# Kernel tuning notes

Hardware: AMD Instinct MI355X
Metric: run time of the kernel (lower is better)

## Reference

```python
import jax, jax.numpy as jnp
import numpy as np

N_NODES = 50000
N_EDGES = 800000
F_DIM = 128
H_DIM = 128


def setup_inputs() -> dict:
    key = jax.random.key(0)
    ks = jax.random.split(key, 14)
    sx = 1.0 / np.sqrt(F_DIM)
    sh = 1.0 / np.sqrt(H_DIM)
    return {
        'x': jax.random.normal(ks[0], (N_NODES, F_DIM), jnp.float32),
        'edge_index': jax.random.randint(ks[1], (2, N_EDGES), 0, N_NODES),
        'edge_weight': jnp.zeros((N_EDGES,), jnp.int32),  # relation ids, all 0 (num_relations=1)
        'h': jax.random.normal(ks[2], (N_NODES, H_DIM), jnp.float32),
        'c': jax.random.normal(ks[3], (N_NODES, H_DIM), jnp.float32),
        # stacked gate params, gate order: i, f, c, o
        'Wx': jax.random.normal(ks[4], (4, F_DIM, H_DIM), jnp.float32) * sx,
        'Wx_root': jax.random.normal(ks[5], (4, F_DIM, H_DIM), jnp.float32) * sx,
        'bx': jax.random.normal(ks[6], (4, H_DIM), jnp.float32) * 0.01,
        'Wh': jax.random.normal(ks[7], (4, H_DIM, H_DIM), jnp.float32) * sh,
        'Wh_root': jax.random.normal(ks[8], (4, H_DIM, H_DIM), jnp.float32) * sh,
        'bh': jax.random.normal(ks[9], (4, H_DIM), jnp.float32) * 0.01,
        'fc_w': jax.random.normal(ks[10], (1, H_DIM), jnp.float32) * sh,
        'fc_b': jax.random.normal(ks[11], (1,), jnp.float32) * 0.01,
    }


def _mean_agg(v, src, dst, n_nodes):
    # scatter-mean of gathered source features onto destination nodes
    s = jax.ops.segment_sum(v[src], dst, num_segments=n_nodes)          # [N, d]
    cnt = jax.ops.segment_sum(jnp.ones(src.shape, v.dtype), dst, num_segments=n_nodes)
    return s / jnp.maximum(cnt, 1.0)[:, None]


def reference(x, edge_index, edge_weight, h, c, Wx, Wx_root, bx, Wh, Wh_root, bh, fc_w, fc_b):
    src, dst = edge_index[0], edge_index[1]
    # single-relation RGCNConv: mean-agg then matmul; aggregation shared across the 4 gates
    agg_x = _mean_agg(x, src, dst, N_NODES)   # [N, F]
    agg_h = _mean_agg(h, src, dst, N_NODES)   # [N, H]
    g = (jnp.einsum('nf,gfh->gnh', agg_x, Wx)
         + jnp.einsum('nf,gfh->gnh', x, Wx_root) + bx[:, None, :]
         + jnp.einsum('nk,gkh->gnh', agg_h, Wh)
         + jnp.einsum('nk,gkh->gnh', h, Wh_root) + bh[:, None, :])  # [4, N, H]
    i_g = jax.nn.sigmoid(g[0])
    f_g = jax.nn.sigmoid(g[1])
    t_g = jnp.tanh(g[2])
    o_g = jax.nn.sigmoid(g[3])
    c_new = f_g * c + i_g * t_g
    h_new = o_g * jnp.tanh(c_new)
    y = jax.nn.relu(h_new) @ fc_w.T + fc_b    # [N, 1]
    return (y, h_new, c_new)
```

## Files before the change

kernel.cpp:

```cpp
#include <hip/hip_runtime.h>
#include <hip/hip_bf16.h>

#define N_NODES 50000
#define N_EDGES 800000
#define FD 128
#define HD 128
#define KTOT 512
#define NTOT 512
#define NRT 391
#define RT_PER_XCD 49
#define SCAN_BLK 1024
#define NSCAN ((N_NODES + SCAN_BLK - 1) / SCAN_BLK)

typedef __attribute__((ext_vector_type(8))) short short8v;
typedef __attribute__((ext_vector_type(8))) __bf16 bf16x8;
typedef __attribute__((ext_vector_type(4))) float f32x4;
typedef __attribute__((ext_vector_type(4))) int i32x4;

__device__ __forceinline__ short f2bf(float f) {
  unsigned u = __builtin_bit_cast(unsigned, f);
  unsigned r = (u + 0x7FFFu + ((u >> 16) & 1u)) >> 16;
  return (short)(r & 0xFFFFu);
}
__device__ __forceinline__ float bf2f(short s) {
  return __builtin_bit_cast(float, ((unsigned)(unsigned short)s) << 16);
}
__device__ __forceinline__ float sigm(float x) {
  return __builtin_amdgcn_rcpf(1.f + __builtin_amdgcn_exp2f(-1.44269504f * x));
}
__device__ __forceinline__ float tanh_(float x) {
  return 1.f - 2.f * __builtin_amdgcn_rcpf(1.f + __builtin_amdgcn_exp2f(2.88539009f * x));
}

__device__ __forceinline__ int swz_col(int c, int r7) {
  return (c & ~63) | (((((c >> 3) & 7) ^ r7)) << 3) | (c & 7);
}

__device__ __forceinline__ void gload_lds16(const void* g, void* l) {
  __builtin_amdgcn_global_load_lds((const __attribute__((address_space(1))) unsigned int*)g,
                                   (__attribute__((address_space(3))) unsigned int*)l, 16, 0, 0);
}

__global__ void k_pre(const float* __restrict__ Wx, const float* __restrict__ Wxr,
                      const float* __restrict__ Wh, const float* __restrict__ Whr,
                      const float* __restrict__ x, const float* __restrict__ h,
                      const int* __restrict__ ei,
                      short* __restrict__ BpackT, short* __restrict__ Apack,
                      int* __restrict__ cnt) {
  int gid = blockIdx.x * 256 + threadIdx.x;
  if (gid < N_EDGES) {
    int d = ei[N_EDGES + gid];
    int r = atomicAdd(&cnt[d], 1);
    ((int*)(Apack + (size_t)(gid >> 6) * KTOT))[gid & 63] = r;
  }
  if (gid < NTOT * KTOT) {
    int col = gid >> 9;
    int k = gid & 511;
    int hb = col >> 7, rem = col & 127;
    int wn = rem >> 6, g = (rem >> 4) & 3, hlow = rem & 15;
    int hid = hb * 32 + wn * 16 + hlow;
    int sel = k >> 7, f = k & 127;
    const float* W = (sel == 0) ? Wx : (sel == 1) ? Wxr : (sel == 2) ? Wh : Whr;
    BpackT[col * KTOT + swz_col(k, col & 7)] = f2bf(W[(g * 128 + f) * 128 + hid]);
  }
  if (gid < N_NODES * 32) {
    int half = gid >= N_NODES * 16;
    int g2 = gid - half * N_NODES * 16;
    int node = g2 >> 4, s = g2 & 15;
    const float* src = (half ? h : x) + (size_t)node * 128 + s * 8;
    f32x4 v0 = *(const f32x4*)(src);
    f32x4 v1 = *(const f32x4*)(src + 4);
    short8v o;
#pragma unroll
    for (int q = 0; q < 4; ++q) { o[q] = f2bf(v0[q]); o[q + 4] = f2bf(v1[q]); }
    int blockbase = 128 + half * 256 + (s >> 3) * 64;
    int slot = (s & 7) ^ (node & 7);
    *(short8v*)(Apack + (size_t)node * KTOT + blockbase + slot * 8) = o;
  }
}

__global__ void k_scanA(const int* __restrict__ cnt, int* __restrict__ bsum) {
  int blk = blockIdx.x, t = threadIdx.x;
  int base = blk * SCAN_BLK + t * 4;
  int s = 0;
  if (base + 3 < N_NODES) {
    i32x4 v = *(const i32x4*)(cnt + base);
    s = v.x + v.y + v.z + v.w;
  }
#pragma unroll
  for (int d = 1; d < 64; d <<= 1) s += __shfl_xor(s, d);
  __shared__ int ws[4];
  if ((t & 63) == 0) ws[t >> 6] = s;
  __syncthreads();
  if (t == 0) bsum[blk] = ws[0] + ws[1] + ws[2] + ws[3];
}

__global__ void k_scanC(const int* __restrict__ cnt, const int* __restrict__ bsum,
                        int* __restrict__ off) {
  __shared__ int sboff[NSCAN];
  int blk = blockIdx.x, t = threadIdx.x;
  if (t < 64) {
    int v = (t < NSCAN) ? bsum[t] : 0;
#pragma unroll
    for (int d = 1; d < 64; d <<= 1) {
      int u = __shfl_up(v, d);
      if (t >= d) v += u;
    }
    if (t < NSCAN) sboff[t] = v;
  }
  __syncthreads();
  int base = blk * SCAN_BLK + t * 4;
  int c0 = 0, c1 = 0, c2 = 0, c3 = 0;
  bool ok = base + 3 < N_NODES;
  if (ok) {
    i32x4 v = *(const i32x4*)(cnt + base);
    c0 = v.x; c1 = v.y; c2 = v.z; c3 = v.w;
  }
  int s = c0 + c1 + c2 + c3;
  int v = s;
#pragma unroll
  for (int d = 1; d < 64; d <<= 1) {
    int u = __shfl_up(v, d);
    if ((t & 63) >= d) v += u;
  }
  __shared__ int wsum[4];
  if ((t & 63) == 63) wsum[t >> 6] = v;
  __syncthreads();
  int wbase = 0;
  for (int w = 0; w < (t >> 6); ++w) wbase += wsum[w];
  int excl = (blk ? sboff[blk - 1] : 0) + wbase + v - s;
  if (ok) {
    i32x4 o = {excl, excl + c0, excl + c0 + c1, excl + c0 + c1 + c2};
    *(i32x4*)(off + base) = o;
  }
  if (blk == 0 && t == 0) off[N_NODES] = N_EDGES;
}

__global__ void k_fill(const int* __restrict__ ei, const int* __restrict__ off,
                       const short* __restrict__ Apack, int* __restrict__ elist) {
  int e = blockIdx.x * 256 + threadIdx.x;
  if (e < N_EDGES) {
    int d = ei[N_EDGES + e];
    int rk = ((const int*)(Apack + (size_t)(e >> 6) * KTOT))[e & 63];
    elist[off[d] + rk] = ei[e];
  }
}

__global__ __launch_bounds__(256) void k_agg_pack(const int* __restrict__ off,
                                                  const int* __restrict__ elist,
                                                  short* __restrict__ Apack) {
  int tid = threadIdx.x;
  int node = blockIdx.x * 4 + (tid >> 6);
  int lane = tid & 63;
  int grp = lane >> 4, l4 = lane & 15;
  int is_h = grp & 1, epair = grp >> 1;
  int b = off[node], e = off[node + 1];
  const int cb = is_h * 256 + 128 + (l4 >> 3) * 64;
  const int sl = l4 & 7;
  float acc[8] = {};
  int j = b;
  for (; j + 8 <= e; j += 8) {
    int s0 = elist[j + epair];
    int s1 = elist[j + 2 + epair];
    int s2 = elist[j + 4 + epair];
    int s3 = elist[j + 6 + epair];
    short8v v0 = *(const short8v*)(Apack + (size_t)s0 * KTOT + cb + ((sl ^ (s0 & 7)) << 3));
    short8v v1 = *(const short8v*)(Apack + (size_t)s1 * KTOT + cb + ((sl ^ (s1 & 7)) << 3));
    short8v v2 = *(const short8v*)(Apack + (size_t)s2 * KTOT + cb + ((sl ^ (s2 & 7)) << 3));
    short8v v3 = *(const short8v*)(Apack + (size_t)s3 * KTOT + cb + ((sl ^ (s3 & 7)) << 3));
#pragma unroll
    for (int q = 0; q < 8; ++q) acc[q] += bf2f(v0[q]);
#pragma unroll
    for (int q = 0; q < 8; ++q) acc[q] += bf2f(v1[q]);
#pragma unroll
    for (int q = 0; q < 8; ++q) acc[q] += bf2f(v2[q]);
#pragma unroll
    for (int q = 0; q < 8; ++q) acc[q] += bf2f(v3[q]);
  }
  for (; j + 2 <= e; j += 2) {
    int s0 = elist[j + epair];
    short8v v0 = *(const short8v*)(Apack + (size_t)s0 * KTOT + cb + ((sl ^ (s0 & 7)) << 3));
#pragma unroll
    for (int q = 0; q < 8; ++q) acc[q] += bf2f(v0[q]);
  }
  if (j < e && epair == 0) {
    int s0 = elist[j];
    short8v v0 = *(const short8v*)(Apack + (size_t)s0 * KTOT + cb + ((sl ^ (s0 & 7)) << 3));
#pragma unroll
    for (int q = 0; q < 8; ++q) acc[q] += bf2f(v0[q]);
  }
#pragma unroll
  for (int q = 0; q < 8; ++q) acc[q] += __shfl_xor(acc[q], 32);
  if (grp < 2) {
    float inv = 1.f / (float)max(e - b, 1);
    int cagg = is_h * 256 + (l4 >> 3) * 64 + ((sl ^ (node & 7)) << 3);
    short8v o;
#pragma unroll
    for (int q = 0; q < 8; ++q) o[q] = f2bf(acc[q] * inv);
    *(short8v*)(Apack + (size_t)node * KTOT + cagg) = o;
  }
}

__global__ __launch_bounds__(512, 4) void k_gemm(
    const short* __restrict__ Apack, const short* __restrict__ BpackT,
    const float* __restrict__ c_in, const float* __restrict__ bx, const float* __restrict__ bh,
    const float* __restrict__ fcw,
    float* __restrict__ hnew, float* __restrict__ cnew, float* __restrict__ ypart) {
  __shared__ short As[2][128 * 64];
  __shared__ short Bs[2][128 * 64];
  const int bid = blockIdx.x;
  const int xcd = bid & 7, q = bid >> 3;
  const int rt = xcd * RT_PER_XCD + (q >> 2);
  const int hb = q & 3;
  if (rt >= NRT) return;
  const int tid = threadIdx.x;
  const int wave = tid >> 6, lane = tid & 63;
  const int l15 = lane & 15, lhi = lane >> 4;
  const int wm = wave & 3, wn = wave >> 2;
  const int row0 = rt * 128;

  const short* Abase = Apack + (size_t)row0 * KTOT;
  const short* Bbase = BpackT + (size_t)hb * 128 * KTOT;
  const int stg_r = tid >> 3;
  const int stg_s = tid & 7;
  const int ldst = (tid & ~63) * 8;

  auto stage = [&](int buf, int k0) {
#pragma unroll
    for (int it = 0; it < 2; ++it) {
      int r = stg_r + it * 64;
      gload_lds16(Abase + (size_t)r * KTOT + k0 + stg_s * 8, &As[buf][ldst + it * 4096]);
      gload_lds16(Bbase + (size_t)r * KTOT + k0 + stg_s * 8, &Bs[buf][ldst + it * 4096]);
    }
  };

  const int rbase = row0 + wm * 32 + lhi * 4;
  const int hid = hb * 32 + wn * 16 + l15;
  float pbi = bx[hid] + bh[hid];
  float pbf = bx[128 + hid] + bh[128 + hid];
  float pbt = bx[256 + hid] + bh[256 + hid];
  float pbo = bx[384 + hid] + bh[384 + hid];
  float pfw = fcw[hid];
  float cpre[2][4];
#pragma unroll
  for (int m = 0; m < 2; ++m)
#pragma unroll
    for (int j = 0; j < 4; ++j) {
      int r = rbase + m * 16 + j;
      cpre[m][j] = (r < N_NODES) ? c_in[(size_t)r * HD + hid] : 0.f;
    }

  f32x4 acc[2][4] = {};

  stage(0, 0);
  __syncthreads();
  int cur = 0;
#pragma unroll
  for (int k0 = 0; k0 < KTOT; k0 += 64) {
    if (k0 + 64 < KTOT) stage(cur ^ 1, k0 + 64);
#pragma unroll
    for (int kk = 0; kk < 2; ++kk) {
      short8v a[2], bfr[4];
      const int sl = ((kk << 2) | lhi) ^ (l15 & 7);
#pragma unroll
      for (int m = 0; m < 2; ++m)
        a[m] = *(const short8v*)(&As[cur][(wm * 32 + m * 16 + l15) * 64 + sl * 8]);
#pragma unroll
      for (int n = 0; n < 4; ++n)
        bfr[n] = *(const short8v*)(&Bs[cur][(wn * 64 + n * 16 + l15) * 64 + sl * 8]);
#pragma unroll
      for (int m = 0; m < 2; ++m)
#pragma unroll
        for (int n = 0; n < 4; ++n)
          acc[m][n] = __builtin_amdgcn_mfma_f32_16x16x32_bf16(
              __builtin_bit_cast(bf16x8, a[m]), __builtin_bit_cast(bf16x8, bfr[n]),
              acc[m][n], 0, 0, 0);
    }
    __syncthreads();
    cur ^= 1;
  }

  float yp[2][4];
#pragma unroll
  for (int m = 0; m < 2; ++m) {
#pragma unroll
    for (int j = 0; j < 4; ++j) {
      int r = rbase + m * 16 + j;
      bool ok = r < N_NODES;
      float ig = sigm(acc[m][0][j] + pbi);
      float fg = sigm(acc[m][1][j] + pbf);
      float tg = tanh_(acc[m][2][j] + pbt);
      float og = sigm(acc[m][3][j] + pbo);
      float cn = fg * cpre[m][j] + ig * tg;
      float hn = og * tanh_(cn);
      if (ok) {
        cnew[(size_t)r * HD + hid] = cn;
        hnew[(size_t)r * HD + hid] = hn;
      }
      yp[m][j] = fmaxf(hn, 0.f) * pfw;
    }
  }
#pragma unroll
  for (int m = 0; m < 2; ++m)
#pragma unroll
    for (int j = 0; j < 4; ++j) {
      float v = yp[m][j];
      v += __shfl_xor(v, 1);
      v += __shfl_xor(v, 2);
      v += __shfl_xor(v, 4);
      v += __shfl_xor(v, 8);
      yp[m][j] = v;
    }
  float* yred = (float*)&As[0][0];
  if (wn == 1 && l15 == 0) {
#pragma unroll
    for (int m = 0; m < 2; ++m)
#pragma unroll
      for (int j = 0; j < 4; ++j)
        yred[wm * 32 + m * 16 + lhi * 4 + j] = yp[m][j];
  }
  __syncthreads();
  if (wn == 0 && l15 == 0) {
#pragma unroll
    for (int m = 0; m < 2; ++m)
#pragma unroll
      for (int j = 0; j < 4; ++j) {
        int r = rbase + m * 16 + j;
        if (r < N_NODES)
          ypart[hb * N_NODES + r] = yp[m][j] + yred[wm * 32 + m * 16 + lhi * 4 + j];
      }
  }
}

__global__ void k_yfinal(const float* __restrict__ ypart, const float* __restrict__ fcb,
                         float* __restrict__ y) {
  int i = blockIdx.x * 256 + threadIdx.x;
  if (i < N_NODES)
    y[i] = fcb[0] + ypart[i] + ypart[N_NODES + i] + ypart[2 * N_NODES + i] + ypart[3 * N_NODES + i];
}

extern "C" void kernel_launch(void* const* d_in, const int* in_sizes, int n_in,
                              void* d_out, int out_size, void* d_ws, size_t ws_size,
                              hipStream_t stream) {
  const float* x   = (const float*)d_in[0];
  const int*   ei  = (const int*)d_in[1];
  const float* h   = (const float*)d_in[3];
  const float* c   = (const float*)d_in[4];
  const float* Wx  = (const float*)d_in[5];
  const float* Wxr = (const float*)d_in[6];
  const float* bx  = (const float*)d_in[7];
  const float* Wh  = (const float*)d_in[8];
  const float* Whr = (const float*)d_in[9];
  const float* bh  = (const float*)d_in[10];
  const float* fcw = (const float*)d_in[11];
  const float* fcb = (const float*)d_in[12];

  float* y    = (float*)d_out;
  float* hnew = y + N_NODES;
  float* cnew = hnew + (size_t)N_NODES * HD;

  char* w = (char*)d_ws;
  auto carve = [&](size_t bytes) {
    char* p = w;
    w += (bytes + 255) & ~(size_t)255;
    return p;
  };
  int* cnt      = (int*)carve((size_t)N_NODES * 4);
  int* off      = (int*)carve((size_t)(N_NODES + 1) * 4);
  int* pos      = (int*)carve((size_t)N_NODES * 4);
  int* elist    = (int*)carve((size_t)N_EDGES * 4);
  short* Apack  = (short*)carve((size_t)N_NODES * KTOT * 2);
  short* BpackT = (short*)carve((size_t)NTOT * KTOT * 2);
  float* ypart  = (float*)carve((size_t)4 * N_NODES * 4);
  int* bsum     = (int*)ypart;
  (void)pos;

  hipMemsetAsync(cnt, 0, (size_t)N_NODES * 4, stream);
  k_pre<<<(N_NODES * 32 + 255) / 256, 256, 0, stream>>>(Wx, Wxr, Wh, Whr, x, h, ei,
                                                        BpackT, Apack, cnt);
  k_scanA<<<NSCAN, 256, 0, stream>>>(cnt, bsum);
  k_scanC<<<NSCAN, 256, 0, stream>>>(cnt, bsum, off);
  k_fill<<<(N_EDGES + 255) / 256, 256, 0, stream>>>(ei, off, Apack, elist);
  k_agg_pack<<<(N_NODES + 3) / 4, 256, 0, stream>>>(off, elist, Apack);
  dim3 gg(8 * RT_PER_XCD * 4);
  k_gemm<<<gg, 512, 0, stream>>>(Apack, BpackT, c, bx, bh, fcw, hnew, cnew, ypart);
  k_yfinal<<<(N_NODES + 255) / 256, 256, 0, stream>>>(ypart, fcb, y);
}
```

Baseline: 170.8 us.

## Retile GEMM to 64-row blocks covering all 512 columns and fuse y reduction

The gate GEMM now gives each block 64 node rows and all 512 output columns (the four gates times 128 hidden units), instead of 128 rows by a quarter of the columns. Each block therefore holds every hidden unit of its rows and can finish the fc reduction in LDS and write y directly, which removes the ypart buffer and the k_yfinal launch. A no longer has to be re-read by four column blocks. In exchange each block stages the full 512x64 B slice per k-step, LDS use grows to about 144 KB per block, and launch bounds drop to 2 blocks per CU, so occupancy and the weight-staging traffic per row change.

After: 191.7 us. 12.2% more time.

```diff
diff --git a/kernel.cpp b/kernel.cpp
--- a/kernel.cpp
+++ b/kernel.cpp
@@ -7,8 +7,9 @@
 #define HD 128
 #define KTOT 512
 #define NTOT 512
-#define NRT 391
-#define RT_PER_XCD 49
+#define BM 64
+#define NBLK ((N_NODES + BM - 1) / BM)
+#define BPX 98
 #define SCAN_BLK 1024
 #define NSCAN ((N_NODES + SCAN_BLK - 1) / SCAN_BLK)
 
@@ -201,56 +202,52 @@
   }
 }
 
-__global__ __launch_bounds__(512, 4) void k_gemm(
+__global__ __launch_bounds__(512, 2) void k_gemm(
     const short* __restrict__ Apack, const short* __restrict__ BpackT,
     const float* __restrict__ c_in, const float* __restrict__ bx, const float* __restrict__ bh,
-    const float* __restrict__ fcw,
-    float* __restrict__ hnew, float* __restrict__ cnew, float* __restrict__ ypart) {
-  __shared__ short As[2][128 * 64];
-  __shared__ short Bs[2][128 * 64];
+    const float* __restrict__ fcw, const float* __restrict__ fcb,
+    float* __restrict__ hnew, float* __restrict__ cnew, float* __restrict__ y) {
+  __shared__ short As[2][BM * 64];
+  __shared__ short Bs[2][NTOT * 64];
   const int bid = blockIdx.x;
   const int xcd = bid & 7, q = bid >> 3;
-  const int rt = xcd * RT_PER_XCD + (q >> 2);
-  const int hb = q & 3;
-  if (rt >= NRT) return;
+  const int blk = xcd * BPX + q;
+  if (blk >= NBLK) return;
   const int tid = threadIdx.x;
   const int wave = tid >> 6, lane = tid & 63;
   const int l15 = lane & 15, lhi = lane >> 4;
-  const int wm = wave & 3, wn = wave >> 2;
-  const int row0 = rt * 128;
+  const int row0 = blk * BM;
 
   const short* Abase = Apack + (size_t)row0 * KTOT;
-  const short* Bbase = BpackT + (size_t)hb * 128 * KTOT;
   const int stg_r = tid >> 3;
   const int stg_s = tid & 7;
   const int ldst = (tid & ~63) * 8;
 
   auto stage = [&](int buf, int k0) {
-#pragma unroll
-    for (int it = 0; it < 2; ++it) {
+    gload_lds16(Abase + (size_t)stg_r * KTOT + k0 + stg_s * 8, &As[buf][ldst]);
+#pragma unroll
+    for (int it = 0; it < 8; ++it) {
       int r = stg_r + it * 64;
-      gload_lds16(Abase + (size_t)r * KTOT + k0 + stg_s * 8, &As[buf][ldst + it * 4096]);
-      gload_lds16(Bbase + (size_t)r * KTOT + k0 + stg_s * 8, &Bs[buf][ldst + it * 4096]);
+      gload_lds16(BpackT + (size_t)r * KTOT + k0 + stg_s * 8, &Bs[buf][ldst + it * 4096]);
     }
   };
 
-  const int rbase = row0 + wm * 32 + lhi * 4;
-  const int hid = hb * 32 + wn * 16 + l15;
+  const int hid = wave * 16 + l15;
   float pbi = bx[hid] + bh[hid];
   float pbf = bx[128 + hid] + bh[128 + hid];
   float pbt = bx[256 + hid] + bh[256 + hid];
   float pbo = bx[384 + hid] + bh[384 + hid];
   float pfw = fcw[hid];
-  float cpre[2][4];
-#pragma unroll
-  for (int m = 0; m < 2; ++m)
+  float cpre[4][4];
+#pragma unroll
+  for (int m = 0; m < 4; ++m)
 #pragma unroll
     for (int j = 0; j < 4; ++j) {
-      int r = rbase + m * 16 + j;
+      int r = row0 + m * 16 + lhi * 4 + j;
       cpre[m][j] = (r < N_NODES) ? c_in[(size_t)r * HD + hid] : 0.f;
     }
 
-  f32x4 acc[2][4] = {};
+  f32x4 acc[4][4] = {};
 
   stage(0, 0);
   __syncthreads();
@@ -260,32 +257,32 @@
     if (k0 + 64 < KTOT) stage(cur ^ 1, k0 + 64);
 #pragma unroll
     for (int kk = 0; kk < 2; ++kk) {
-      short8v a[2], bfr[4];
+      short8v a[4], bfr[4];
       const int sl = ((kk << 2) | lhi) ^ (l15 & 7);
 #pragma unroll
-      for (int m = 0; m < 2; ++m)
-        a[m] = *(const short8v*)(&As[cur][(wm * 32 + m * 16 + l15) * 64 + sl * 8]);
-#pragma unroll
-      for (int n = 0; n < 4; ++n)
-        bfr[n] = *(const short8v*)(&Bs[cur][(wn * 64 + n * 16 + l15) * 64 + sl * 8]);
-#pragma unroll
-      for (int m = 0; m < 2; ++m)
-#pragma unroll
-        for (int n = 0; n < 4; ++n)
-          acc[m][n] = __builtin_amdgcn_mfma_f32_16x16x32_bf16(
-              __builtin_bit_cast(bf16x8, a[m]), __builtin_bit_cast(bf16x8, bfr[n]),
-              acc[m][n], 0, 0, 0);
+      for (int m = 0; m < 4; ++m)
+        a[m] = *(const short8v*)(&As[cur][(m * 16 + l15) * 64 + sl * 8]);
+#pragma unroll
+      for (int g = 0; g < 4; ++g)
+        bfr[g] = *(const short8v*)(&Bs[cur][(wave * 64 + g * 16 + l15) * 64 + sl * 8]);
+#pragma unroll
+      for (int m = 0; m < 4; ++m)
+#pragma unroll
+        for (int g = 0; g < 4; ++g)
+          acc[m][g] = __builtin_amdgcn_mfma_f32_16x16x32_bf16(
+              __builtin_bit_cast(bf16x8, a[m]), __builtin_bit_cast(bf16x8, bfr[g]),
+              acc[m][g], 0, 0, 0);
     }
     __syncthreads();
     cur ^= 1;
   }
 
-  float yp[2][4];
-#pragma unroll
-  for (int m = 0; m < 2; ++m) {
+  float yp[4][4];
+#pragma unroll
+  for (int m = 0; m < 4; ++m) {
 #pragma unroll
     for (int j = 0; j < 4; ++j) {
-      int r = rbase + m * 16 + j;
+      int r = row0 + m * 16 + lhi * 4 + j;
       bool ok = r < N_NODES;
       float ig = sigm(acc[m][0][j] + pbi);
       float fg = sigm(acc[m][1][j] + pbf);
@@ -301,7 +298,7 @@
     }
   }
 #pragma unroll
-  for (int m = 0; m < 2; ++m)
+  for (int m = 0; m < 4; ++m)
 #pragma unroll
     for (int j = 0; j < 4; ++j) {
       float v = yp[m][j];
@@ -312,31 +309,23 @@
       yp[m][j] = v;
     }
   float* yred = (float*)&As[0][0];
-  if (wn == 1 && l15 == 0) {
-#pragma unroll
-    for (int m = 0; m < 2; ++m)
+  if (l15 == 0) {
+#pragma unroll
+    for (int m = 0; m < 4; ++m)
 #pragma unroll
       for (int j = 0; j < 4; ++j)
-        yred[wm * 32 + m * 16 + lhi * 4 + j] = yp[m][j];
-  }
-  __syncthreads();
-  if (wn == 0 && l15 == 0) {
-#pragma unroll
-    for (int m = 0; m < 2; ++m)
-#pragma unroll
-      for (int j = 0; j < 4; ++j) {
-        int r = rbase + m * 16 + j;
-        if (r < N_NODES)
-          ypart[hb * N_NODES + r] = yp[m][j] + yred[wm * 32 + m * 16 + lhi * 4 + j];
-      }
-  }
-}
-
-__global__ void k_yfinal(const float* __restrict__ ypart, const float* __restrict__ fcb,
-                         float* __restrict__ y) {
-  int i = blockIdx.x * 256 + threadIdx.x;
-  if (i < N_NODES)
-    y[i] = fcb[0] + ypart[i] + ypart[N_NODES + i] + ypart[2 * N_NODES + i] + ypart[3 * N_NODES + i];
+        yred[wave * 64 + m * 16 + lhi * 4 + j] = yp[m][j];
+  }
+  __syncthreads();
+  if (wave == 0) {
+    int r = row0 + lane;
+    if (r < N_NODES) {
+      float v = fcb[0];
+#pragma unroll
+      for (int w = 0; w < 8; ++w) v += yred[w * 64 + lane];
+      y[r] = v;
+    }
+  }
 }
 
 extern "C" void kernel_launch(void* const* d_in, const int* in_sizes, int n_in,
@@ -382,7 +371,5 @@
   k_scanC<<<NSCAN, 256, 0, stream>>>(cnt, bsum, off);
   k_fill<<<(N_EDGES + 255) / 256, 256, 0, stream>>>(ei, off, Apack, elist);
   k_agg_pack<<<(N_NODES + 3) / 4, 256, 0, stream>>>(off, elist, Apack);
-  dim3 gg(8 * RT_PER_XCD * 4);
-  k_gemm<<<gg, 512, 0, stream>>>(Apack, BpackT, c, bx, bh, fcw, hnew, cnew, ypart);
-  k_yfinal<<<(N_NODES + 255) / 256, 256, 0, stream>>>(ypart, fcb, y);
-}
+  k_gemm<<<8 * BPX, 512, 0, stream>>>(Apack, BpackT, c, bx, bh, fcw, fcb, hnew, cnew, y);
+}
```
